# Performance work log

Hardware: AMD Instinct MI355X
Metric: run time of the kernel (lower is better)

The kernel has to match this reference:

```python
import jax, jax.numpy as jnp
import numpy as np

IN_CH = 1024   # backbone channels
N_T = 81       # n_targets (COCO classes + bg)
K = 7          # PSROI grid size
H = 100        # feature map height
WID = 100      # feature map width
R = 1024       # number of regions
S = 2          # bilinear sampling points per bin edge (PSROIAlign-style average)


def setup_inputs() -> dict:
    key = jax.random.key(0)
    k1, k2, k3 = jax.random.split(key, 3)
    x = jax.random.normal(k1, (IN_CH, H, WID), dtype=jnp.float32)
    # regions: fractional (i, j, h, w) = (center_y, center_x, height, width) in [0,1]
    regions = jax.random.uniform(k2, (R, 4), dtype=jnp.float32)
    conv_w = jax.random.normal(k3, (N_T * K * K, IN_CH), dtype=jnp.float32) * 0.02
    conv_b = jnp.zeros((N_T * K * K,), dtype=jnp.float32)
    return {"x": x, "regions": regions, "conv_w": conv_w, "conv_b": conv_b}


def _bilinear_pool(map_thw, ys, xs):
    """Average of bilinear samples of one bin's score map.

    map_thw: (T, H, W) score map for this (u, v) bin's channel group.
    ys: (R, S) sample row coords.  xs: (R, S) sample col coords.
    Returns (R, T): per-region average-pooled bin value.
    """
    Hm, Wm = map_thw.shape[1], map_thw.shape[2]
    ys = jnp.clip(ys, 0.0, Hm - 1)
    xs = jnp.clip(xs, 0.0, Wm - 1)
    y0 = jnp.floor(ys)
    x0 = jnp.floor(xs)
    y0i = y0.astype(jnp.int32)
    x0i = x0.astype(jnp.int32)
    y1i = jnp.minimum(y0i + 1, Hm - 1)
    x1i = jnp.minimum(x0i + 1, Wm - 1)
    wy1 = ys - y0
    wy0 = 1.0 - wy1
    wx1 = xs - x0
    wx0 = 1.0 - wx1

    def g(yi, xi):  # gather (T, R, S, S)
        return map_thw[:, yi[:, :, None], xi[:, None, :]]

    v = (g(y0i, x0i) * (wy0[:, :, None] * wx0[:, None, :])
         + g(y0i, x1i) * (wy0[:, :, None] * wx1[:, None, :])
         + g(y1i, x0i) * (wy1[:, :, None] * wx0[:, None, :])
         + g(y1i, x1i) * (wy1[:, :, None] * wx1[:, None, :]))
    return v.mean((2, 3)).T  # (R, T)


def reference(x, regions, conv_w, conv_b):
    # 1x1 conv score map: (n_targets*k^2, H, W)
    sm = jnp.einsum('oc,chw->ohw', conv_w, x) + conv_b[:, None, None]
    sm = sm.reshape(N_T, K, K, H, WID)  # (T, ky, kx, H, W) position-sensitive groups

    # region geometry (fractional center/size -> absolute feature-map coords)
    top = (regions[:, 0] - regions[:, 2] * 0.5) * H     # (R,)
    left = (regions[:, 1] - regions[:, 3] * 0.5) * WID  # (R,)
    bh = regions[:, 2] * H / K                          # bin height
    bw = regions[:, 3] * WID / K                        # bin width

    off = (jnp.arange(S, dtype=jnp.float32) + 0.5) / S  # (S,) sample offsets in bin
    bins = jnp.arange(K, dtype=jnp.float32)             # (K,)
    ys = top[:, None, None] + (bins[None, :, None] + off[None, None, :]) * bh[:, None, None]   # (R,K,S)
    xs = left[:, None, None] + (bins[None, :, None] + off[None, None, :]) * bw[:, None, None]  # (R,K,S)

    # vmap over the k x k position-sensitive bins; bin (u,v) reads channel group (:,u,v)
    inner = jax.vmap(_bilinear_pool, in_axes=(1, None, 1))  # over kx: sm axis, xs axis
    outer = jax.vmap(inner, in_axes=(1, 1, None))           # over ky: sm axis, ys axis
    pooled = outer(sm, ys, xs)  # (K, K, R, T)

    # pooled.mean(-1).mean(-1) over the k x k grid
    scores = pooled.mean((0, 1))  # (R, T)
    return scores
```

## Files before the change

kernel.cpp:

```cpp
#include <hip/hip_runtime.h>
#include <cstddef>

#define IN_CH 1024
#define NT    81
#define KGRID 7
#define NBINS 49
#define HH    100
#define WW    100
#define NPIX  (HH*WW)
#define NREG  1024
#define COLB  82
#define NCOL  (NBINS*COLB)
#define NPADW 4096
#define SBIN  84
#define SROWB (NBINS*SBIN)
#define NG    8
#define NSC   2560
#define PXB   ((NPIX + 31) / 32)
#define PXG   (PXB * (IN_CH / 128))
#define PREPG (PXG + NPADW)

typedef unsigned short ushortT;
typedef short bf16x8 __attribute__((ext_vector_type(8)));
typedef float f32x4  __attribute__((ext_vector_type(4)));

static __device__ __forceinline__ unsigned short f2bf(float f) {
    unsigned int u = __builtin_bit_cast(unsigned int, f);
    return (unsigned short)((u + 0x7fffu + ((u >> 16) & 1u)) >> 16);
}

static __device__ __forceinline__ void gld_lds16(const ushortT* g, ushortT* l) {
    __builtin_amdgcn_global_load_lds(
        (__attribute__((address_space(1))) void*)(unsigned long long)(uintptr_t)g,
        (__attribute__((address_space(3))) void*)(unsigned int)(unsigned long long)(uintptr_t)l,
        16, 0, 0);
}

__global__ __launch_bounds__(256) void prep_fused(const float* __restrict__ x,
                                                  ushortT* __restrict__ xbT,
                                                  const float* __restrict__ conv_w,
                                                  ushortT* __restrict__ Wr) {
    __shared__ float tile[128][33];
    const int tid = threadIdx.x;
    const int bid = blockIdx.x;
    if (bid < PXG) {
        const int p0 = (bid % PXB) * 32;
        const int c0 = (bid / PXB) * 128;
        const int pl = tid & 31;
        const int cg = tid >> 5;
        const int p = p0 + pl;
#pragma unroll
        for (int it = 0; it < 16; ++it) {
            const int c = it * 8 + cg;
            tile[c][pl] = (p < NPIX) ? x[(size_t)(c0 + c) * NPIX + p] : 0.0f;
        }
        __syncthreads();
#pragma unroll
        for (int pass = 0; pass < 2; ++pass) {
            const int pix = pass * 16 + (tid >> 4);
            const int cb  = (tid & 15) * 8;
            if (p0 + pix < NPIX) {
                uint4 pk;
                pk.x = (unsigned int)f2bf(tile[cb + 0][pix]) | ((unsigned int)f2bf(tile[cb + 1][pix]) << 16);
                pk.y = (unsigned int)f2bf(tile[cb + 2][pix]) | ((unsigned int)f2bf(tile[cb + 3][pix]) << 16);
                pk.z = (unsigned int)f2bf(tile[cb + 4][pix]) | ((unsigned int)f2bf(tile[cb + 5][pix]) << 16);
                pk.w = (unsigned int)f2bf(tile[cb + 6][pix]) | ((unsigned int)f2bf(tile[cb + 7][pix]) << 16);
                *(uint4*)(xbT + (size_t)(p0 + pix) * IN_CH + c0 + cb) = pk;
            }
        }
    } else {
        const int row = bid - PXG;
        const int bin = row / COLB;
        const int t   = row - bin * COLB;
        const int c   = tid * 4;
        uint2 pk; pk.x = 0; pk.y = 0;
        if (bin < NBINS && t < NT) {
            const float4 v = *(const float4*)(conv_w + ((size_t)(t * NBINS + bin)) * IN_CH + c);
            pk.x = (unsigned int)f2bf(v.x) | ((unsigned int)f2bf(v.y) << 16);
            pk.y = (unsigned int)f2bf(v.z) | ((unsigned int)f2bf(v.w) << 16);
        }
        *(uint2*)(Wr + (size_t)row * IN_CH + c) = pk;
    }
}

__global__ __launch_bounds__(256) void gemm_sm(const ushortT* __restrict__ xbT,
                                               const ushortT* __restrict__ Wr,
                                               unsigned char* __restrict__ sm,
                                               float* __restrict__ scales) {
    __shared__ ushortT a_lds[128 * 32];
    __shared__ ushortT b_lds[128 * 32];
    const int tid  = threadIdx.x;
    const int lane = tid & 63;
    const int w    = tid >> 6;
    const int wm   = w & 1;
    const int wn   = w >> 1;
    const int n0   = blockIdx.x * 128;
    const int p0   = blockIdx.y * 128;

    const int srow0 = w * 32 + (lane >> 2);
    const int scol  = (lane & 3) * 8;
    int ap0 = p0 + srow0;      if (ap0 > NPIX - 1) ap0 = NPIX - 1;
    int ap1 = p0 + srow0 + 16; if (ap1 > NPIX - 1) ap1 = NPIX - 1;
    const ushortT* ag0 = xbT + (size_t)ap0 * IN_CH + scol;
    const ushortT* ag1 = xbT + (size_t)ap1 * IN_CH + scol;
    const ushortT* bg0 = Wr + (size_t)(n0 + srow0) * IN_CH + scol;
    const ushortT* bg1 = Wr + (size_t)(n0 + srow0 + 16) * IN_CH + scol;
    ushortT* al0 = a_lds + (w * 32) * 32;
    ushortT* al1 = a_lds + (w * 32 + 16) * 32;
    ushortT* bl0 = b_lds + (w * 32) * 32;
    ushortT* bl1 = b_lds + (w * 32 + 16) * 32;

    const int m_lane = lane & 15;
    const int k0     = (lane >> 4) * 8;

    f32x4 acc[4][4];
#pragma unroll
    for (int mt = 0; mt < 4; ++mt)
#pragma unroll
        for (int nt = 0; nt < 4; ++nt) acc[mt][nt] = (f32x4){0.f, 0.f, 0.f, 0.f};

    for (int kc = 0; kc < IN_CH / 32; ++kc) {
        __syncthreads();
        gld_lds16(ag0, al0);
        gld_lds16(ag1, al1);
        gld_lds16(bg0, bl0);
        gld_lds16(bg1, bl1);
        ag0 += 32; ag1 += 32; bg0 += 32; bg1 += 32;
        __syncthreads();

        bf16x8 af[4], bf[4];
#pragma unroll
        for (int mt = 0; mt < 4; ++mt)
            af[mt] = *(const bf16x8*)(a_lds + (wm * 64 + mt * 16 + m_lane) * 32 + k0);
#pragma unroll
        for (int nt = 0; nt < 4; ++nt)
            bf[nt] = *(const bf16x8*)(b_lds + (wn * 64 + nt * 16 + m_lane) * 32 + k0);
#pragma unroll
        for (int mt = 0; mt < 4; ++mt)
#pragma unroll
            for (int nt = 0; nt < 4; ++nt)
                acc[mt][nt] = __builtin_amdgcn_mfma_f32_16x16x32_bf16(af[mt], bf[nt], acc[mt][nt], 0, 0, 0);
    }

    float am = 0.0f;
#pragma unroll
    for (int mt = 0; mt < 4; ++mt)
#pragma unroll
        for (int nt = 0; nt < 4; ++nt)
#pragma unroll
            for (int rg = 0; rg < 4; ++rg)
                am = fmaxf(am, fabsf(acc[mt][nt][rg]));
    __syncthreads();
    float* red = (float*)a_lds;
    red[tid] = am;
    __syncthreads();
#pragma unroll
    for (int s = 128; s > 0; s >>= 1) {
        if (tid < s) red[tid] = fmaxf(red[tid], red[tid + s]);
        __syncthreads();
    }
    const float amax = fmaxf(red[0], 1e-30f);
    const float inv  = 127.0f / amax;
    if (tid == 0) scales[blockIdx.y * 32 + blockIdx.x] = amax * (1.0f / 127.0f);

    const int prow_base = p0 + wm * 64 + (lane >> 4) * 4;
    const int ncol_base = n0 + wn * 64 + m_lane;
    int  coloff[4];
    bool cok[4];
#pragma unroll
    for (int nt = 0; nt < 4; ++nt) {
        const int n = ncol_base + nt * 16;
        cok[nt] = (n < NCOL);
        coloff[nt] = n + 2 * (n / COLB);
    }
#pragma unroll
    for (int mt = 0; mt < 4; ++mt) {
#pragma unroll
        for (int rg = 0; rg < 4; ++rg) {
            const int p = prow_base + mt * 16 + rg;
            if (p < NPIX) {
                unsigned char* rowp = sm + (size_t)p * SROWB;
#pragma unroll
                for (int nt = 0; nt < 4; ++nt)
                    if (cok[nt]) {
                        const int q = __float2int_rn(acc[mt][nt][rg] * inv);
                        rowp[coloff[nt]] = (unsigned char)(signed char)q;
                    }
            }
        }
    }
}

__global__ __launch_bounds__(256) void pool_kernel(const unsigned char* __restrict__ sm,
                                                   const float* __restrict__ scales,
                                                   const float* __restrict__ regions,
                                                   const float* __restrict__ conv_b,
                                                   float* __restrict__ out) {
    __shared__ int   rowo[28]; __shared__ float roww[28];
    __shared__ int   coli[28]; __shared__ float colw[28];
    __shared__ int   pofs[120];
    __shared__ float pw[120];
    __shared__ int   pptb[120];
    __shared__ int   pnb[120];
    __shared__ float part[40][100];
    const int tid = threadIdx.x;
    const int r = blockIdx.x;
    const int g = blockIdx.y;

    if (tid < 28) {
        const float4 reg = *(const float4*)(regions + (size_t)r * 4);
        const float top = (reg.x - reg.z * 0.5f) * (float)HH;
        const float bh  = reg.z * ((float)HH / (float)KGRID);
        const int u = tid >> 2, i = tid & 3;
        const int s = i >> 1, hi = i & 1;
        float y = top + ((float)u + ((float)s + 0.5f) * 0.5f) * bh;
        y = fminf(fmaxf(y, 0.0f), (float)(HH - 1));
        const float y0f = floorf(y);
        const int y0 = (int)y0f;
        const float wy1 = y - y0f;
        rowo[tid] = (hi ? min(y0 + 1, HH - 1) : y0) * WW;
        roww[tid] = hi ? wy1 : (1.0f - wy1);
    } else if (tid >= 32 && tid < 60) {
        const float4 reg = *(const float4*)(regions + (size_t)r * 4);
        const float left = (reg.y - reg.w * 0.5f) * (float)WW;
        const float bw   = reg.w * ((float)WW / (float)KGRID);
        const int idx = tid - 32;
        const int v = idx >> 2, j = idx & 3;
        const int s = j >> 1, hi = j & 1;
        float xx = left + ((float)v + ((float)s + 0.5f) * 0.5f) * bw;
        xx = fminf(fmaxf(xx, 0.0f), (float)(WW - 1));
        const float x0f = floorf(xx);
        const int x0 = (int)x0f;
        const float wx1 = xx - x0f;
        coli[idx] = hi ? min(x0 + 1, WW - 1) : x0;
        colw[idx] = hi ? wx1 : (1.0f - wx1);
    }
    __syncthreads();
    if (tid < 120) {
        if (tid < 98) {
            const int tt = g * 98 + tid;
            const int bin = tt >> 4, tap = tt & 15;
            const int u = bin / KGRID, v = bin - u * KGRID;
            const int i = tap >> 2, j = tap & 3;
            const int pix = rowo[u * 4 + i] + coli[v * 4 + j];
            pofs[tid] = pix * SROWB + bin * SBIN;
            pw[tid]   = roww[u * 4 + i] * colw[v * 4 + j] * (1.0f / 196.0f);
            pptb[tid] = (pix >> 7) * 32;
            pnb[tid]  = bin * COLB;
        } else {
            pofs[tid] = 0;
            pw[tid]   = 0.0f;
            pptb[tid] = 0;
            pnb[tid]  = 0;
        }
    }
    __syncthreads();

    const int lane = tid & 63, w = tid >> 6;
    const int sub  = lane / 6;
    const int cg   = lane - sub * 6;
    if (sub < 10) {
        const int str = w * 10 + sub;
        uint4 v[3];
#pragma unroll
        for (int it = 0; it < 3; ++it)
            v[it] = *(const uint4*)(sm + pofs[it * 40 + str] + cg * 16);

        float acc[16];
#pragma unroll
        for (int ch = 0; ch < 16; ++ch) acc[ch] = 0.0f;
#pragma unroll
        for (int it = 0; it < 3; ++it) {
            const int l  = it * 40 + str;
            const float wt = pw[l];
            const int nb  = pnb[l] + cg * 16;
            const int nt0 = nb >> 7;
            const int rr  = nb & 127;
            const float s0 = scales[pptb[l] + nt0];
            const float s1 = scales[pptb[l] + nt0 + 1];
            const float w0 = wt * s0, w1 = wt * s1;
            const unsigned int uu[4] = {v[it].x, v[it].y, v[it].z, v[it].w};
#pragma unroll
            for (int b = 0; b < 4; ++b) {
#pragma unroll
                for (int k = 0; k < 4; ++k) {
                    const int ch = b * 4 + k;
                    const int q = (int)(signed char)((uu[b] >> (k * 8)) & 0xff);
                    acc[ch] += ((rr < 128 - ch) ? w0 : w1) * (float)q;
                }
            }
        }
#pragma unroll
        for (int b = 0; b < 4; ++b) {
            float4 p4;
            p4.x = acc[b * 4]; p4.y = acc[b * 4 + 1];
            p4.z = acc[b * 4 + 2]; p4.w = acc[b * 4 + 3];
            *(float4*)&part[str][cg * 16 + b * 4] = p4;
        }
    }
    __syncthreads();
    if (tid < NT) {
        float vv = 0.f;
#pragma unroll
        for (int s = 0; s < 40; ++s) vv += part[s][tid];
        if (g == 0) {
            float bsum = 0.f;
            for (int bin = 0; bin < NBINS; ++bin) bsum += conv_b[tid * NBINS + bin];
            vv += bsum * (1.0f / (float)NBINS);
        }
        atomicAdd(out + (size_t)r * NT + tid, vv);
    }
}

__global__ __launch_bounds__(256) void xpose_kernel(const float* __restrict__ x,
                                                    float* __restrict__ xt) {
    __shared__ float tile[32][33];
    const int p0 = blockIdx.x * 32;
    const int c0 = blockIdx.y * 32;
    const int tx = threadIdx.x;
    const int ty = threadIdx.y;
#pragma unroll
    for (int k = 0; k < 32; k += 8) {
        const int p = p0 + tx;
        if (p < NPIX) tile[ty + k][tx] = x[(size_t)(c0 + ty + k) * NPIX + p];
    }
    __syncthreads();
#pragma unroll
    for (int k = 0; k < 32; k += 8) {
        const int p = p0 + ty + k;
        if (p < NPIX) xt[(size_t)p * IN_CH + (c0 + tx)] = tile[tx][ty + k];
    }
}

template <bool XPOSED>
__global__ __launch_bounds__(256) void psroi_kernel(
    const float* __restrict__ xsrc, const float* __restrict__ regions,
    const float* __restrict__ conv_w, const float* __restrict__ conv_b,
    float* __restrict__ out) {
    __shared__ float w_lds[32 * 96];
    __shared__ float g_lds[32 * 64];
    __shared__ int   rowoff[64][4];
    __shared__ float rowwf[64][4];
    __shared__ int   colidx[64][4];
    __shared__ float colwf[64][4];
    const int tid = threadIdx.x;
    const int bin = blockIdx.x >> 4;
    const int rg  = blockIdx.x & 15;
    const int u = bin / KGRID, v = bin % KGRID;
    const int r0 = rg * 64;
    if (tid < 64) {
        const float4 reg = *(const float4*)(regions + (size_t)(r0 + tid) * 4);
        const float top  = (reg.x - reg.z * 0.5f) * (float)HH;
        const float left = (reg.y - reg.w * 0.5f) * (float)WW;
        const float bh = reg.z * ((float)HH / (float)KGRID);
        const float bw = reg.w * ((float)WW / (float)KGRID);
        const float scale = 1.0f / 196.0f;
#pragma unroll
        for (int s = 0; s < 2; s++) {
            const float off = (s + 0.5f) * 0.5f;
            float yy = top + ((float)u + off) * bh;
            yy = fminf(fmaxf(yy, 0.0f), (float)(HH - 1));
            const float y0f = floorf(yy);
            const int y0 = (int)y0f;
            const float wy1 = yy - y0f;
            rowoff[tid][2 * s] = y0 * WW;
            rowoff[tid][2 * s + 1] = min(y0 + 1, HH - 1) * WW;
            rowwf[tid][2 * s] = (1.0f - wy1) * scale;
            rowwf[tid][2 * s + 1] = wy1 * scale;
            float xx = left + ((float)v + off) * bw;
            xx = fminf(fmaxf(xx, 0.0f), (float)(WW - 1));
            const float x0f = floorf(xx);
            const int x0 = (int)x0f;
            const float wx1 = xx - x0f;
            colidx[tid][2 * s] = x0;
            colidx[tid][2 * s + 1] = min(x0 + 1, WW - 1);
            colwf[tid][2 * s] = 1.0f - wx1;
            colwf[tid][2 * s + 1] = wx1;
        }
    }
    const int ri = tid & 15, tq = tid >> 4, rb = tid >> 2, cq = tid & 3;
    float acc[4][6];
#pragma unroll
    for (int m = 0; m < 4; m++)
#pragma unroll
        for (int k = 0; k < 6; k++) acc[m][k] = 0.0f;
    for (int chunk = 0; chunk < IN_CH / 32; chunk++) {
        const int c0 = chunk * 32;
        __syncthreads();
#pragma unroll
        for (int it = 0; it < 12; it++) {
            const int idx = it * 256 + tid;
            const int t = idx >> 5, c = idx & 31;
            float val = 0.0f;
            if (t < NT) val = conv_w[(size_t)(t * NBINS + bin) * IN_CH + c0 + c];
            w_lds[c * 96 + t] = val;
        }
        const int cbase = c0 + cq * 8;
        float g8[8];
#pragma unroll
        for (int cc = 0; cc < 8; cc++) g8[cc] = 0.0f;
#pragma unroll
        for (int i = 0; i < 4; i++) {
            const int ro = rowoff[rb][i];
            const float wy = rowwf[rb][i];
#pragma unroll
            for (int j = 0; j < 4; j++) {
                const int pix = ro + colidx[rb][j];
                const float wv = wy * colwf[rb][j];
                if (XPOSED) {
                    const float4* p = (const float4*)(xsrc + (size_t)pix * IN_CH + cbase);
                    const float4 a = p[0]; const float4 b = p[1];
                    g8[0] += wv * a.x; g8[1] += wv * a.y; g8[2] += wv * a.z; g8[3] += wv * a.w;
                    g8[4] += wv * b.x; g8[5] += wv * b.y; g8[6] += wv * b.z; g8[7] += wv * b.w;
                } else {
#pragma unroll
                    for (int cc = 0; cc < 8; cc++)
                        g8[cc] += wv * xsrc[(size_t)(cbase + cc) * NPIX + pix];
                }
            }
        }
#pragma unroll
        for (int cc = 0; cc < 8; cc++) g_lds[(cq * 8 + cc) * 64 + rb] = g8[cc];
        __syncthreads();
#pragma unroll 4
        for (int c = 0; c < 32; c++) {
            float wv[6];
#pragma unroll
            for (int k = 0; k < 6; k++) wv[k] = w_lds[c * 96 + tq * 6 + k];
            const float4 gq = *(const float4*)&g_lds[c * 64 + ri * 4];
            const float gm[4] = {gq.x, gq.y, gq.z, gq.w};
#pragma unroll
            for (int m = 0; m < 4; m++)
#pragma unroll
                for (int k = 0; k < 6; k++) acc[m][k] += gm[m] * wv[k];
        }
    }
    const float invK2 = 1.0f / 49.0f;
#pragma unroll
    for (int k = 0; k < 6; k++) {
        const int t = tq * 6 + k;
        if (t < NT) {
            const float bterm = conv_b[t * NBINS + bin] * invK2;
#pragma unroll
            for (int m = 0; m < 4; m++) {
                const int rr = r0 + ri * 4 + m;
                atomicAdd(&out[(size_t)rr * NT + t], acc[m][k] + bterm);
            }
        }
    }
}

extern "C" void kernel_launch(void* const* d_in, const int* in_sizes, int n_in,
                              void* d_out, int out_size, void* d_ws, size_t ws_size,
                              hipStream_t stream) {
    const float* x       = (const float*)d_in[0];
    const float* regions = (const float*)d_in[1];
    const float* conv_w  = (const float*)d_in[2];
    const float* conv_b  = (const float*)d_in[3];
    float* out = (float*)d_out;

    const size_t sz_xbT = (size_t)NPIX * IN_CH * 2;
    const size_t sz_Wr  = (size_t)NPADW * IN_CH * 2;
    const size_t sz_sm  = (size_t)NPIX * SROWB + 256;
    const size_t sz_sc  = (size_t)NSC * sizeof(float);
    const size_t need   = sz_xbT + sz_Wr + sz_sm + sz_sc;

    if (ws_size >= need) {
        ushortT* xbT = (ushortT*)d_ws;
        ushortT* Wr  = (ushortT*)((char*)d_ws + sz_xbT);
        unsigned char* sm = (unsigned char*)d_ws + sz_xbT + sz_Wr;
        float* scales = (float*)((char*)d_ws + sz_xbT + sz_Wr + sz_sm);
        hipMemsetAsync(out, 0, (size_t)out_size * sizeof(float), stream);
        prep_fused<<<dim3(PREPG), 256, 0, stream>>>(x, xbT, conv_w, Wr);
        gemm_sm<<<dim3(NPADW / 128, (NPIX + 127) / 128), 256, 0, stream>>>(xbT, Wr, sm, scales);
        pool_kernel<<<dim3(NREG, NG), 256, 0, stream>>>(sm, scales, regions, conv_b, out);
    } else {
        hipMemsetAsync(out, 0, (size_t)out_size * sizeof(float), stream);
        const size_t xt_bytes = (size_t)NPIX * IN_CH * sizeof(float);
        const dim3 mainGrid(NBINS * 16);
        if (ws_size >= xt_bytes) {
            float* xt = (float*)d_ws;
            xpose_kernel<<<dim3((NPIX + 31) / 32, IN_CH / 32), dim3(32, 8), 0, stream>>>(x, xt);
            psroi_kernel<true><<<mainGrid, 256, 0, stream>>>(xt, regions, conv_w, conv_b, out);
        } else {
            psroi_kernel<false><<<mainGrid, 256, 0, stream>>>(x, regions, conv_w, conv_b, out);
        }
    }
}
```

Before: 230.3 us.

## Quantize conv GEMM inputs to int8 with per-pixel and per-row scales

Replaces the bf16 1x1-conv GEMM with an int8 MFMA GEMM (16x16x64 i8). A new amax pass computes a per-pixel scale for x, and weight prep computes a per-output-row scale. The GEMM dequantizes the int32 accumulators with both scales before the existing per-tile int8 requantization of the score map. This halves operand bytes and doubles the K per MFMA, at the cost of an extra full read of x and lower precision on both inputs.

```diff
diff --git a/kernel.cpp b/kernel.cpp
--- a/kernel.cpp
+++ b/kernel.cpp
@@ -21,25 +21,52 @@
 #define PREPG (PXG + NPADW)
 
 typedef unsigned short ushortT;
-typedef short bf16x8 __attribute__((ext_vector_type(8)));
-typedef float f32x4  __attribute__((ext_vector_type(4)));
+typedef unsigned char  u8;
+typedef int i32x4 __attribute__((ext_vector_type(4)));
 
 static __device__ __forceinline__ unsigned short f2bf(float f) {
     unsigned int u = __builtin_bit_cast(unsigned int, f);
     return (unsigned short)((u + 0x7fffu + ((u >> 16) & 1u)) >> 16);
 }
 
-static __device__ __forceinline__ void gld_lds16(const ushortT* g, ushortT* l) {
+static __device__ __forceinline__ void gld_lds16(const void* g, void* l) {
     __builtin_amdgcn_global_load_lds(
         (__attribute__((address_space(1))) void*)(unsigned long long)(uintptr_t)g,
         (__attribute__((address_space(3))) void*)(unsigned int)(unsigned long long)(uintptr_t)l,
         16, 0, 0);
 }
 
+__global__ __launch_bounds__(256) void amax_x(const float* __restrict__ x,
+                                              float* __restrict__ sxa,
+                                              float* __restrict__ inv_sxa) {
+    __shared__ float red[4][64];
+    const int tid = threadIdx.x;
+    const int pl = tid & 63, cg = tid >> 6;
+    const int p = blockIdx.x * 64 + pl;
+    float am = 1e-30f;
+    if (p < NPIX) {
+        for (int c = cg; c < IN_CH; c += 4)
+            am = fmaxf(am, fabsf(x[(size_t)c * NPIX + p]));
+    }
+    red[cg][pl] = am;
+    __syncthreads();
+    if (tid < 64) {
+        const float m = fmaxf(fmaxf(red[0][tid], red[1][tid]),
+                              fmaxf(red[2][tid], red[3][tid]));
+        const int pp = blockIdx.x * 64 + tid;
+        if (pp < NPIX) {
+            sxa[pp]     = m * (1.0f / 127.0f);
+            inv_sxa[pp] = 127.0f / m;
+        }
+    }
+}
+
 __global__ __launch_bounds__(256) void prep_fused(const float* __restrict__ x,
-                                                  ushortT* __restrict__ xbT,
+                                                  u8* __restrict__ xq,
+                                                  const float* __restrict__ inv_sxa,
                                                   const float* __restrict__ conv_w,
-                                                  ushortT* __restrict__ Wr) {
+                                                  u8* __restrict__ Wq,
+                                                  float* __restrict__ sxb) {
     __shared__ float tile[128][33];
     const int tid = threadIdx.x;
     const int bid = blockIdx.x;
@@ -55,40 +82,64 @@
             tile[c][pl] = (p < NPIX) ? x[(size_t)(c0 + c) * NPIX + p] : 0.0f;
         }
         __syncthreads();
-#pragma unroll
-        for (int pass = 0; pass < 2; ++pass) {
-            const int pix = pass * 16 + (tid >> 4);
-            const int cb  = (tid & 15) * 8;
-            if (p0 + pix < NPIX) {
-                uint4 pk;
-                pk.x = (unsigned int)f2bf(tile[cb + 0][pix]) | ((unsigned int)f2bf(tile[cb + 1][pix]) << 16);
-                pk.y = (unsigned int)f2bf(tile[cb + 2][pix]) | ((unsigned int)f2bf(tile[cb + 3][pix]) << 16);
-                pk.z = (unsigned int)f2bf(tile[cb + 4][pix]) | ((unsigned int)f2bf(tile[cb + 5][pix]) << 16);
-                pk.w = (unsigned int)f2bf(tile[cb + 6][pix]) | ((unsigned int)f2bf(tile[cb + 7][pix]) << 16);
-                *(uint4*)(xbT + (size_t)(p0 + pix) * IN_CH + c0 + cb) = pk;
+        const int pix = tid >> 3;
+        const int cb  = (tid & 7) * 16;
+        const int pp = p0 + pix;
+        if (pp < NPIX) {
+            const float inv = inv_sxa[pp];
+            uint4 pk;
+            unsigned int w[4];
+#pragma unroll
+            for (int q = 0; q < 4; ++q) {
+                unsigned int acc = 0;
+#pragma unroll
+                for (int j = 0; j < 4; ++j) {
+                    const int v = __float2int_rn(tile[cb + q * 4 + j][pix] * inv);
+                    acc |= ((unsigned int)(v & 0xff)) << (j * 8);
+                }
+                w[q] = acc;
             }
+            pk.x = w[0]; pk.y = w[1]; pk.z = w[2]; pk.w = w[3];
+            *(uint4*)(xq + (size_t)pp * IN_CH + c0 + cb) = pk;
         }
     } else {
         const int row = bid - PXG;
         const int bin = row / COLB;
         const int t   = row - bin * COLB;
         const int c   = tid * 4;
-        uint2 pk; pk.x = 0; pk.y = 0;
-        if (bin < NBINS && t < NT) {
-            const float4 v = *(const float4*)(conv_w + ((size_t)(t * NBINS + bin)) * IN_CH + c);
-            pk.x = (unsigned int)f2bf(v.x) | ((unsigned int)f2bf(v.y) << 16);
-            pk.y = (unsigned int)f2bf(v.z) | ((unsigned int)f2bf(v.w) << 16);
-        }
-        *(uint2*)(Wr + (size_t)row * IN_CH + c) = pk;
-    }
-}
-
-__global__ __launch_bounds__(256) void gemm_sm(const ushortT* __restrict__ xbT,
-                                               const ushortT* __restrict__ Wr,
-                                               unsigned char* __restrict__ sm,
+        float4 v; v.x = 0.f; v.y = 0.f; v.z = 0.f; v.w = 0.f;
+        if (bin < NBINS && t < NT)
+            v = *(const float4*)(conv_w + ((size_t)(t * NBINS + bin)) * IN_CH + c);
+        float am = fmaxf(fmaxf(fabsf(v.x), fabsf(v.y)), fmaxf(fabsf(v.z), fabsf(v.w)));
+        float* red = (float*)tile;
+        red[tid] = am;
+        __syncthreads();
+#pragma unroll
+        for (int s = 128; s > 0; s >>= 1) {
+            if (tid < s) red[tid] = fmaxf(red[tid], red[tid + s]);
+            __syncthreads();
+        }
+        const float amax = fmaxf(red[0], 1e-30f);
+        const float inv  = 127.0f / amax;
+        if (tid == 0) sxb[row] = amax * (1.0f / 127.0f);
+        const int q0 = __float2int_rn(v.x * inv);
+        const int q1 = __float2int_rn(v.y * inv);
+        const int q2 = __float2int_rn(v.z * inv);
+        const int q3 = __float2int_rn(v.w * inv);
+        const unsigned int pk = (unsigned int)(q0 & 0xff) | ((unsigned int)(q1 & 0xff) << 8) |
+                                ((unsigned int)(q2 & 0xff) << 16) | ((unsigned int)(q3 & 0xff) << 24);
+        *(unsigned int*)(Wq + (size_t)row * IN_CH + c) = pk;
+    }
+}
+
+__global__ __launch_bounds__(256) void gemm_sm(const u8* __restrict__ xq,
+                                               const u8* __restrict__ Wq,
+                                               const float* __restrict__ sxa,
+                                               const float* __restrict__ sxb,
+                                               u8* __restrict__ sm,
                                                float* __restrict__ scales) {
-    __shared__ ushortT a_lds[128 * 32];
-    __shared__ ushortT b_lds[128 * 32];
+    __shared__ u8 a_lds[8192];
+    __shared__ u8 b_lds[8192];
     const int tid  = threadIdx.x;
     const int lane = tid & 63;
     const int w    = tid >> 6;
@@ -97,50 +148,62 @@
     const int n0   = blockIdx.x * 128;
     const int p0   = blockIdx.y * 128;
 
-    const int srow0 = w * 32 + (lane >> 2);
-    const int scol  = (lane & 3) * 8;
-    int ap0 = p0 + srow0;      if (ap0 > NPIX - 1) ap0 = NPIX - 1;
-    int ap1 = p0 + srow0 + 16; if (ap1 > NPIX - 1) ap1 = NPIX - 1;
-    const ushortT* ag0 = xbT + (size_t)ap0 * IN_CH + scol;
-    const ushortT* ag1 = xbT + (size_t)ap1 * IN_CH + scol;
-    const ushortT* bg0 = Wr + (size_t)(n0 + srow0) * IN_CH + scol;
-    const ushortT* bg1 = Wr + (size_t)(n0 + srow0 + 16) * IN_CH + scol;
-    ushortT* al0 = a_lds + (w * 32) * 32;
-    ushortT* al1 = a_lds + (w * 32 + 16) * 32;
-    ushortT* bl0 = b_lds + (w * 32) * 32;
-    ushortT* bl1 = b_lds + (w * 32 + 16) * 32;
-
-    const int m_lane = lane & 15;
-    const int k0     = (lane >> 4) * 8;
-
-    f32x4 acc[4][4];
+    const int m  = lane & 15;
+    const int g  = lane >> 4;
+    int ar0 = p0 + w * 32 + m;       if (ar0 > NPIX - 1) ar0 = NPIX - 1;
+    int ar1 = p0 + w * 32 + 16 + m;  if (ar1 > NPIX - 1) ar1 = NPIX - 1;
+    const u8* ag0 = xq + (size_t)ar0 * IN_CH + g * 16;
+    const u8* ag1 = xq + (size_t)ar1 * IN_CH + g * 16;
+    const u8* bg0 = Wq + (size_t)(n0 + w * 32 + m) * IN_CH + g * 16;
+    const u8* bg1 = Wq + (size_t)(n0 + w * 32 + 16 + m) * IN_CH + g * 16;
+    u8* al0 = a_lds + (w * 2) * 1024 + lane * 16;
+    u8* al1 = a_lds + (w * 2 + 1) * 1024 + lane * 16;
+    u8* bl0 = b_lds + (w * 2) * 1024 + lane * 16;
+    u8* bl1 = b_lds + (w * 2 + 1) * 1024 + lane * 16;
+
+    i32x4 acc[4][4];
 #pragma unroll
     for (int mt = 0; mt < 4; ++mt)
 #pragma unroll
-        for (int nt = 0; nt < 4; ++nt) acc[mt][nt] = (f32x4){0.f, 0.f, 0.f, 0.f};
-
-    for (int kc = 0; kc < IN_CH / 32; ++kc) {
+        for (int nt = 0; nt < 4; ++nt) acc[mt][nt] = (i32x4){0, 0, 0, 0};
+
+    for (int kc = 0; kc < IN_CH / 64; ++kc) {
         __syncthreads();
         gld_lds16(ag0, al0);
         gld_lds16(ag1, al1);
         gld_lds16(bg0, bl0);
         gld_lds16(bg1, bl1);
-        ag0 += 32; ag1 += 32; bg0 += 32; bg1 += 32;
-        __syncthreads();
-
-        bf16x8 af[4], bf[4];
+        ag0 += 64; ag1 += 64; bg0 += 64; bg1 += 64;
+        __syncthreads();
+
+        i32x4 af[4], bf[4];
 #pragma unroll
         for (int mt = 0; mt < 4; ++mt)
-            af[mt] = *(const bf16x8*)(a_lds + (wm * 64 + mt * 16 + m_lane) * 32 + k0);
+            af[mt] = *(const i32x4*)(a_lds + (wm * 4 + mt) * 1024 + lane * 16);
 #pragma unroll
         for (int nt = 0; nt < 4; ++nt)
-            bf[nt] = *(const bf16x8*)(b_lds + (wn * 64 + nt * 16 + m_lane) * 32 + k0);
+            bf[nt] = *(const i32x4*)(b_lds + (wn * 4 + nt) * 1024 + lane * 16);
 #pragma unroll
         for (int mt = 0; mt < 4; ++mt)
 #pragma unroll
             for (int nt = 0; nt < 4; ++nt)
-                acc[mt][nt] = __builtin_amdgcn_mfma_f32_16x16x32_bf16(af[mt], bf[nt], acc[mt][nt], 0, 0, 0);
-    }
+                acc[mt][nt] = __builtin_amdgcn_mfma_i32_16x16x64_i8(af[mt], bf[nt], acc[mt][nt], 0, 0, 0);
+    }
+
+    const int prow_base = p0 + wm * 64 + (lane >> 4) * 4;
+    const int ncol_base = n0 + wn * 64 + m;
+    float sb4[4];
+#pragma unroll
+    for (int nt = 0; nt < 4; ++nt) sb4[nt] = sxb[ncol_base + nt * 16];
+    float sa4[4][4];
+#pragma unroll
+    for (int mt = 0; mt < 4; ++mt)
+#pragma unroll
+        for (int rg = 0; rg < 4; ++rg) {
+            int p = prow_base + mt * 16 + rg;
+            if (p > NPIX - 1) p = NPIX - 1;
+            sa4[mt][rg] = sxa[p];
+        }
 
     float am = 0.0f;
 #pragma unroll
@@ -149,7 +212,7 @@
         for (int nt = 0; nt < 4; ++nt)
 #pragma unroll
             for (int rg = 0; rg < 4; ++rg)
-                am = fmaxf(am, fabsf(acc[mt][nt][rg]));
+                am = fmaxf(am, fabsf((float)acc[mt][nt][rg] * sa4[mt][rg] * sb4[nt]));
     __syncthreads();
     float* red = (float*)a_lds;
     red[tid] = am;
@@ -163,8 +226,6 @@
     const float inv  = 127.0f / amax;
     if (tid == 0) scales[blockIdx.y * 32 + blockIdx.x] = amax * (1.0f / 127.0f);
 
-    const int prow_base = p0 + wm * 64 + (lane >> 4) * 4;
-    const int ncol_base = n0 + wn * 64 + m_lane;
     int  coloff[4];
     bool cok[4];
 #pragma unroll
@@ -179,19 +240,20 @@
         for (int rg = 0; rg < 4; ++rg) {
             const int p = prow_base + mt * 16 + rg;
             if (p < NPIX) {
-                unsigned char* rowp = sm + (size_t)p * SROWB;
+                u8* rowp = sm + (size_t)p * SROWB;
 #pragma unroll
                 for (int nt = 0; nt < 4; ++nt)
                     if (cok[nt]) {
-                        const int q = __float2int_rn(acc[mt][nt][rg] * inv);
-                        rowp[coloff[nt]] = (unsigned char)(signed char)q;
+                        const float fv = (float)acc[mt][nt][rg] * sa4[mt][rg] * sb4[nt];
+                        const int q = __float2int_rn(fv * inv);
+                        rowp[coloff[nt]] = (u8)(signed char)q;
                     }
             }
         }
     }
 }
 
-__global__ __launch_bounds__(256) void pool_kernel(const unsigned char* __restrict__ sm,
+__global__ __launch_bounds__(256) void pool_kernel(const u8* __restrict__ sm,
                                                    const float* __restrict__ scales,
                                                    const float* __restrict__ regions,
                                                    const float* __restrict__ conv_b,
@@ -459,20 +521,28 @@
     const float* conv_b  = (const float*)d_in[3];
     float* out = (float*)d_out;
 
-    const size_t sz_xbT = (size_t)NPIX * IN_CH * 2;
-    const size_t sz_Wr  = (size_t)NPADW * IN_CH * 2;
+    const size_t sz_xq  = (size_t)NPIX * IN_CH;
+    const size_t sz_Wq  = (size_t)NPADW * IN_CH;
+    const size_t sz_sxa = 10048 * sizeof(float);
+    const size_t sz_isxa= 10048 * sizeof(float);
+    const size_t sz_sxb = (size_t)NPADW * sizeof(float);
+    const size_t sz_sc  = (size_t)NSC * sizeof(float);
     const size_t sz_sm  = (size_t)NPIX * SROWB + 256;
-    const size_t sz_sc  = (size_t)NSC * sizeof(float);
-    const size_t need   = sz_xbT + sz_Wr + sz_sm + sz_sc;
+    const size_t need   = sz_xq + sz_Wq + sz_sxa + sz_isxa + sz_sxb + sz_sc + sz_sm;
 
     if (ws_size >= need) {
-        ushortT* xbT = (ushortT*)d_ws;
-        ushortT* Wr  = (ushortT*)((char*)d_ws + sz_xbT);
-        unsigned char* sm = (unsigned char*)d_ws + sz_xbT + sz_Wr;
-        float* scales = (float*)((char*)d_ws + sz_xbT + sz_Wr + sz_sm);
+        char* base = (char*)d_ws;
+        u8*    xq      = (u8*)base;                       base += sz_xq;
+        u8*    Wq      = (u8*)base;                       base += sz_Wq;
+        float* sxa     = (float*)base;                    base += sz_sxa;
+        float* inv_sxa = (float*)base;                    base += sz_isxa;
+        float* sxb     = (float*)base;                    base += sz_sxb;
+        float* scales  = (float*)base;                    base += sz_sc;
+        u8*    sm      = (u8*)base;
         hipMemsetAsync(out, 0, (size_t)out_size * sizeof(float), stream);
-        prep_fused<<<dim3(PREPG), 256, 0, stream>>>(x, xbT, conv_w, Wr);
-        gemm_sm<<<dim3(NPADW / 128, (NPIX + 127) / 128), 256, 0, stream>>>(xbT, Wr, sm, scales);
+        amax_x<<<dim3((NPIX + 63) / 64), 256, 0, stream>>>(x, sxa, inv_sxa);
+        prep_fused<<<dim3(PREPG), 256, 0, stream>>>(x, xq, inv_sxa, conv_w, Wq, sxb);
+        gemm_sm<<<dim3(NPADW / 128, (NPIX + 127) / 128), 256, 0, stream>>>(xq, Wq, sxa, sxb, sm, scales);
         pool_kernel<<<dim3(NREG, NG), 256, 0, stream>>>(sm, scales, regions, conv_b, out);
     } else {
         hipMemsetAsync(out, 0, (size_t)out_size * sizeof(float), stream);
```

Result: slower. 266.3 us (+15.6%).
